# Kernel tuning notes

Hardware: AMD Instinct MI355X
Metric: run time of the kernel (lower is better)

## Reference

```python
import jax, jax.numpy as jnp
import numpy as np
import math

TABLE_SIZE = 524288      # 2**19 entries per level
NUM_LEVELS = 16
MIN_RES = 16
MAX_RES = 1024
FEATURE_DIM = 2
N_POINTS = 1 << 20
HASH_PRIME = np.uint32(2654435761)  # standard Instant-NGP spatial hash prime


def _hash(vertex, table_size, hash_offset):
    # vertex: (N, L, 2) int32 grid coords; returns (N, L) int32 table indices
    v = vertex.astype(jnp.uint32)
    h = v[..., 0] ^ (v[..., 1] * HASH_PRIME)          # uint32 wraparound mul
    return (h % jnp.uint32(table_size)).astype(jnp.int32) + hash_offset


def setup_inputs() -> dict:
    key = jax.random.key(0)
    kx, kt = jax.random.split(key)
    x = jax.random.uniform(kx, (N_POINTS, 2), dtype=jnp.float32)  # points in [0,1)^2
    # nn.initializers.uniform(scale=1e-4): U[0, 1e-4)
    hash_table = jax.random.uniform(
        kt, (TABLE_SIZE * NUM_LEVELS, FEATURE_DIM), dtype=jnp.float32) * 1e-4
    return {"x": x, "hash_table": hash_table}


def reference(x, hash_table):
    levels = jnp.arange(NUM_LEVELS)
    growth = math.exp((math.log(MAX_RES) - math.log(MIN_RES)) / (NUM_LEVELS - 1))
    scalings = jnp.floor(MIN_RES * (growth ** levels.astype(jnp.float32)))  # (L,)
    hash_offset = (levels * TABLE_SIZE).astype(jnp.int32)                   # (L,)

    scaled = x[:, None, :] * scalings[None, :, None]   # (N, L, 2)
    scaled_c = jnp.ceil(scaled).astype(jnp.int32)
    scaled_f = jnp.floor(scaled).astype(jnp.int32)
    off = scaled - scaled_f                            # (N, L, 2) bilinear weights

    v0 = scaled_c                                                          # (cx, cy)
    v1 = jnp.stack([scaled_c[..., 0], scaled_f[..., 1]], axis=-1)          # (cx, fy)
    v2 = jnp.stack([scaled_f[..., 0], scaled_c[..., 1]], axis=-1)          # (fx, cy)
    v3 = scaled_f                                                          # (fx, fy)

    f0 = hash_table[_hash(v0, TABLE_SIZE, hash_offset)]  # (N, L, F)
    f1 = hash_table[_hash(v1, TABLE_SIZE, hash_offset)]
    f2 = hash_table[_hash(v2, TABLE_SIZE, hash_offset)]
    f3 = hash_table[_hash(v3, TABLE_SIZE, hash_offset)]

    ox = off[..., 0:1]  # (N, L, 1)
    oy = off[..., 1:2]
    f03 = f0 * ox + f3 * (1.0 - ox)
    f12 = f1 * ox + f2 * (1.0 - ox)
    enc = f03 * oy + f12 * (1.0 - oy)                  # (N, L, F)
    # per-point layout matches ravel(transpose(F,L)->(L,F)): level-major
    return enc.reshape(x.shape[0], NUM_LEVELS * FEATURE_DIM)
```

## Files before the change

kernel.cpp:

```cpp
#include <hip/hip_runtime.h>

#define TS 524288u
#define PRIME 2654435761u
#define NPTS 1048576u
#define MASK (TS - 1u)
#define NBUK 4096u
#define CAP 320u
#define OVF_CAP 8192u

#define WS_CURSOR   0u
#define WS_OVFCNT   16384u
#define WS_OVF_XY   16640u
#define WS_OVF_IDX  82176u
#define WS_XYBUF    131072u
#define WS_IDXBUF   10616832u
#define WS_NEED     15859712u

typedef float vfloat4 __attribute__((ext_vector_type(4)));

__device__ __constant__ float c_scale[16] = {
    16.f, 21.f, 27.f, 36.f, 48.f, 64.f, 84.f, 111.f,
    147.f, 194.f, 256.f, 337.f, 445.f, 588.f, 776.f, 1024.f
};

#define W0 17
#define W1 22
#define W2 28
#define W3 37
#define B0 0
#define B1 (B0 + W0*W0)
#define B2 (B1 + W1*W1)
#define B3 (B2 + W2*W2)
#define NSTAGE (B3 + W3*W3)

__device__ __forceinline__ unsigned bucket_of(float2 xy) {
    unsigned bx = (unsigned)(xy.x * 64.0f); if (bx > 63u) bx = 63u;
    unsigned by = (unsigned)(xy.y * 64.0f); if (by > 63u) by = 63u;
    return by * 64u + bx;
}

__device__ __forceinline__ void enc_level(
    float2 xy, unsigned l, const float2* __restrict__ tab,
    float& ex, float& ey)
{
    float s = c_scale[l];
    float sx = xy.x * s, sy = xy.y * s;
    float fxf = floorf(sx), fyf = floorf(sy);
    float cxf = ceilf(sx),  cyf = ceilf(sy);
    float ox = sx - fxf, oy = sy - fyf;
    unsigned fx = (unsigned)(int)fxf, fy = (unsigned)(int)fyf;
    unsigned cx = (unsigned)(int)cxf, cy = (unsigned)(int)cyf;
    unsigned hcy = cy * PRIME, hfy = fy * PRIME;
    unsigned base = l << 19;
    float2 f0 = tab[((cx ^ hcy) & MASK) | base];
    float2 f1 = tab[((cx ^ hfy) & MASK) | base];
    float2 f2 = tab[((fx ^ hcy) & MASK) | base];
    float2 f3 = tab[((fx ^ hfy) & MASK) | base];
    float wox = 1.0f - ox, woy = 1.0f - oy;
    float f03x = f0.x * ox + f3.x * wox;
    float f03y = f0.y * ox + f3.y * wox;
    float f12x = f1.x * ox + f2.x * wox;
    float f12y = f1.y * ox + f2.y * wox;
    ex = f03x * oy + f12x * woy;
    ey = f03y * oy + f12y * woy;
}

__global__ __launch_bounds__(256) void init_kernel(
    unsigned* __restrict__ cursor, unsigned* __restrict__ ovf_cnt)
{
    unsigned t = blockIdx.x * 256u + threadIdx.x;
    if (t < NBUK) cursor[t] = t * CAP;
    if (t == 0u) *ovf_cnt = 0u;
}

__global__ __launch_bounds__(256) void sort_kernel(
    const float2* __restrict__ x,
    unsigned* __restrict__ cursor,
    unsigned* __restrict__ ovf_cnt,
    float2* __restrict__ ovf_xy,
    unsigned* __restrict__ ovf_idx,
    float2* __restrict__ xybuf,
    unsigned* __restrict__ idxbuf)
{
    __shared__ unsigned lhist[NBUK];
    __shared__ unsigned lbase_cap[NBUK];
    unsigned tid = threadIdx.x;
    unsigned cbase = blockIdx.x * 1024u;

    for (unsigned j = tid; j < NBUK; j += 256u) lhist[j] = 0u;
    __syncthreads();

    float2 pxy[4];
#pragma unroll
    for (int k = 0; k < 4; ++k) {
        float2 xy = x[cbase + tid + (unsigned)k * 256u];
        pxy[k] = xy;
        atomicAdd(&lhist[bucket_of(xy)], 1u);
    }
    __syncthreads();

    for (unsigned j = tid; j < NBUK; j += 256u) {
        unsigned c = lhist[j];
        unsigned base = 0u, take = 0u;
        if (c) {
            base = atomicAdd(&cursor[j], c);
            unsigned prior = base - j * CAP;
            unsigned avail = (prior >= CAP) ? 0u : (CAP - prior);
            take = (c < avail) ? c : avail;
        }
        lbase_cap[j] = (base << 9) | take;
        lhist[j] = 0u;
    }
    __syncthreads();

#pragma unroll
    for (int k = 0; k < 4; ++k) {
        float2 xy = pxy[k];
        unsigned b = bucket_of(xy);
        unsigned idx = cbase + tid + (unsigned)k * 256u;
        unsigned loff = atomicAdd(&lhist[b], 1u);
        unsigned bc = lbase_cap[b];
        unsigned take = bc & 511u;
        if (loff < take) {
            unsigned pos = (bc >> 9) + loff;
            xybuf[pos] = xy;
            idxbuf[pos] = idx;
        } else {
            unsigned o = atomicAdd(ovf_cnt, 1u);
            if (o < OVF_CAP) { ovf_xy[o] = xy; ovf_idx[o] = idx; }
        }
    }
}

__global__ __launch_bounds__(512) void encode_kernel(
    const float2* __restrict__ xybuf,
    const unsigned* __restrict__ idxbuf,
    const unsigned* __restrict__ cursor,
    const float2* __restrict__ tab,
    vfloat4* __restrict__ out)
{
    __shared__ float2 lds[NSTAGE];
    unsigned tid = threadIdx.x;

#define STAGE(L, W, B)                                                  \
    for (unsigned i = tid; i < (unsigned)((W)*(W)); i += 512u) {        \
        unsigned vy = i / (unsigned)(W), vx = i % (unsigned)(W);        \
        unsigned h = ((vx ^ (vy * PRIME)) & MASK) | ((unsigned)(L) << 19); \
        lds[(B) + i] = tab[h];                                          \
    }
    STAGE(0, W0, B0)
    STAGE(1, W1, B1)
    STAGE(2, W2, B2)
    STAGE(3, W3, B3)
#undef STAGE
    __syncthreads();

    unsigned wave = tid >> 6;
    unsigned lane = tid & 63u;
    unsigned lq   = lane & 3u;
    unsigned s0   = lane >> 2;
    unsigned b    = blockIdx.x * 8u + wave;
    unsigned total = cursor[b] - b * CAP;
    unsigned cnt  = (total < CAP) ? total : CAP;
    unsigned l0   = lq << 2;
    unsigned pbase = b * CAP;

    const unsigned Wk[4] = { W0, W1, W2, W3 };
    const unsigned Bk[4] = { B0, B1, B2, B3 };

    for (unsigned s = s0; s < cnt; s += 16u) {
        float2 xy   = xybuf[pbase + s];
        unsigned idx = idxbuf[pbase + s];
        vfloat4 r[2];

        if (lq == 0u) {
#pragma unroll
            for (int k = 0; k < 4; ++k) {
                float sc = c_scale[k];
                float sx = xy.x * sc, sy = xy.y * sc;
                float fxf = floorf(sx), fyf = floorf(sy);
                float cxf = ceilf(sx),  cyf = ceilf(sy);
                float ox = sx - fxf, oy = sy - fyf;
                unsigned fx = (unsigned)(int)fxf, fy = (unsigned)(int)fyf;
                unsigned cx = (unsigned)(int)cxf, cy = (unsigned)(int)cyf;
                unsigned w = Wk[k], bb = Bk[k];
                float2 f0 = lds[bb + cy * w + cx];
                float2 f1 = lds[bb + fy * w + cx];
                float2 f2 = lds[bb + cy * w + fx];
                float2 f3 = lds[bb + fy * w + fx];
                float wox = 1.0f - ox, woy = 1.0f - oy;
                float f03x = f0.x * ox + f3.x * wox;
                float f03y = f0.y * ox + f3.y * wox;
                float f12x = f1.x * ox + f2.x * wox;
                float f12y = f1.y * ox + f2.y * wox;
                float ex = f03x * oy + f12x * woy;
                float ey = f03y * oy + f12y * woy;
                if ((k & 1) == 0) { r[k >> 1].x = ex; r[k >> 1].y = ey; }
                else              { r[k >> 1].z = ex; r[k >> 1].w = ey; }
            }
        } else {
#pragma unroll
            for (int k = 0; k < 4; ++k) {
                float ex, ey;
                enc_level(xy, l0 + (unsigned)k, tab, ex, ey);
                if ((k & 1) == 0) { r[k >> 1].x = ex; r[k >> 1].y = ey; }
                else              { r[k >> 1].z = ex; r[k >> 1].w = ey; }
            }
        }

        unsigned o = idx * 8u + lq * 2u;
        __builtin_nontemporal_store(r[0], &out[o]);
        __builtin_nontemporal_store(r[1], &out[o + 1]);
    }
}

__global__ __launch_bounds__(256) void fixup_kernel(
    const unsigned* __restrict__ ovf_cnt,
    const float2* __restrict__ ovf_xy,
    const unsigned* __restrict__ ovf_idx,
    const float2* __restrict__ tab,
    vfloat4* __restrict__ out)
{
    unsigned n = *ovf_cnt; if (n > OVF_CAP) n = OVF_CAP;
    unsigned stride = gridDim.x * 256u;
    for (unsigned p = blockIdx.x * 256u + threadIdx.x; p < n; p += stride) {
        float2 xy = ovf_xy[p];
        unsigned idx = ovf_idx[p];
        vfloat4 acc[8];
#pragma unroll
        for (int l = 0; l < 16; ++l) {
            float ex, ey;
            enc_level(xy, (unsigned)l, tab, ex, ey);
            if ((l & 1) == 0) { acc[l >> 1].x = ex; acc[l >> 1].y = ey; }
            else              { acc[l >> 1].z = ex; acc[l >> 1].w = ey; }
        }
#pragma unroll
        for (int q = 0; q < 8; ++q) out[idx * 8u + (unsigned)q] = acc[q];
    }
}

__global__ __launch_bounds__(256) void hashenc_kernel(
    const float2* __restrict__ x,
    const float2* __restrict__ tab,
    vfloat4* __restrict__ out,
    unsigned pts_per_block)
{
    __shared__ float2 lds[NSTAGE];
    unsigned tid = threadIdx.x;

#define STAGE(L, W, B)                                                  \
    for (unsigned i = tid; i < (unsigned)((W)*(W)); i += 256u) {        \
        unsigned vy = i / (unsigned)(W), vx = i % (unsigned)(W);        \
        unsigned h = ((vx ^ (vy * PRIME)) & MASK) | ((unsigned)(L) << 19); \
        lds[(B) + i] = tab[h];                                          \
    }
    STAGE(0, W0, B0)
    STAGE(1, W1, B1)
    STAGE(2, W2, B2)
    STAGE(3, W3, B3)
#undef STAGE
    __syncthreads();

    const unsigned lq = tid & 3u;
    const unsigned lane_p = tid >> 2;
    const unsigned l0 = lq << 2;
    const unsigned bs = blockIdx.x * pts_per_block;
    unsigned be = bs + pts_per_block;
    if (be > NPTS) be = NPTS;

    const unsigned Wk[4] = { W0, W1, W2, W3 };
    const unsigned Bk[4] = { B0, B1, B2, B3 };

    for (unsigned p = bs + lane_p; p < be; p += 64u) {
        float2 xy = x[p];
        vfloat4 r[2];

        if (lq == 0u) {
#pragma unroll
            for (int k = 0; k < 4; ++k) {
                float s = c_scale[k];
                float sx = xy.x * s, sy = xy.y * s;
                float fxf = floorf(sx), fyf = floorf(sy);
                float cxf = ceilf(sx),  cyf = ceilf(sy);
                float ox = sx - fxf, oy = sy - fyf;
                unsigned fx = (unsigned)(int)fxf, fy = (unsigned)(int)fyf;
                unsigned cx = (unsigned)(int)cxf, cy = (unsigned)(int)cyf;
                unsigned w = Wk[k], b = Bk[k];
                float2 f0 = lds[b + cy * w + cx];
                float2 f1 = lds[b + fy * w + cx];
                float2 f2 = lds[b + cy * w + fx];
                float2 f3 = lds[b + fy * w + fx];
                float wox = 1.0f - ox, woy = 1.0f - oy;
                float f03x = f0.x * ox + f3.x * wox;
                float f03y = f0.y * ox + f3.y * wox;
                float f12x = f1.x * ox + f2.x * wox;
                float f12y = f1.y * ox + f2.y * wox;
                float ex = f03x * oy + f12x * woy;
                float ey = f03y * oy + f12y * woy;
                if ((k & 1) == 0) { r[k >> 1].x = ex; r[k >> 1].y = ey; }
                else              { r[k >> 1].z = ex; r[k >> 1].w = ey; }
            }
        } else {
#pragma unroll
            for (int k = 0; k < 4; ++k) {
                float ex, ey;
                enc_level(xy, l0 + (unsigned)k, tab, ex, ey);
                if ((k & 1) == 0) { r[k >> 1].x = ex; r[k >> 1].y = ey; }
                else              { r[k >> 1].z = ex; r[k >> 1].w = ey; }
            }
        }

        unsigned o = p * 8u + lq * 2u;
        __builtin_nontemporal_store(r[0], &out[o]);
        __builtin_nontemporal_store(r[1], &out[o + 1]);
    }
}

extern "C" void kernel_launch(void* const* d_in, const int* in_sizes, int n_in,
                              void* d_out, int out_size, void* d_ws, size_t ws_size,
                              hipStream_t stream)
{
    const float2* x   = (const float2*)d_in[0];
    const float2* tab = (const float2*)d_in[1];
    vfloat4* out = (vfloat4*)d_out;

    if (d_ws != nullptr && ws_size >= (size_t)WS_NEED) {
        char* ws = (char*)d_ws;
        unsigned* cursor  = (unsigned*)(ws + WS_CURSOR);
        unsigned* ovf_cnt = (unsigned*)(ws + WS_OVFCNT);
        float2*   ovf_xy  = (float2*)  (ws + WS_OVF_XY);
        unsigned* ovf_idx = (unsigned*)(ws + WS_OVF_IDX);
        float2*   xybuf   = (float2*)  (ws + WS_XYBUF);
        unsigned* idxbuf  = (unsigned*)(ws + WS_IDXBUF);

        init_kernel<<<16, 256, 0, stream>>>(cursor, ovf_cnt);
        sort_kernel<<<1024, 256, 0, stream>>>(x, cursor, ovf_cnt, ovf_xy,
                                              ovf_idx, xybuf, idxbuf);
        encode_kernel<<<NBUK / 8, 512, 0, stream>>>(xybuf, idxbuf, cursor, tab, out);
        fixup_kernel<<<8, 256, 0, stream>>>(ovf_cnt, ovf_xy, ovf_idx, tab, out);
    } else {
        const unsigned n_blocks = 1536u;
        const unsigned ppb = (NPTS + n_blocks - 1u) / n_blocks;
        hashenc_kernel<<<n_blocks, 256, 0, stream>>>(x, tab, out, ppb);
    }
}
```

Before: 314.1 us.

## Stage per-bucket hash tiles for all levels in LDS, enlarge sort blocks

Each wave in the encode kernel now gathers, for its own spatial bucket, the local window of hashed table entries for all 16 levels into LDS. All levels then interpolate from LDS instead of doing random global gathers, which previously happened for levels 4-15. The sort kernel also handles 4096 points per 512-thread block, cutting global cursor atomics. In exchange the staging gathers add upfront work per bucket and LDS use rises to about 65KB per block, which can lower occupancy.

```diff
diff --git a/kernel.cpp b/kernel.cpp
--- a/kernel.cpp
+++ b/kernel.cpp
@@ -22,6 +22,14 @@
     16.f, 21.f, 27.f, 36.f, 48.f, 64.f, 84.f, 111.f,
     147.f, 194.f, 256.f, 337.f, 445.f, 588.f, 776.f, 1024.f
 };
+
+__device__ __constant__ unsigned c_lvl[16] = {
+    (0u  <<5)|3u,  (9u  <<5)|3u,  (18u <<5)|3u,  (27u <<5)|3u,
+    (36u <<5)|3u,  (45u <<5)|3u,  (54u <<5)|4u,  (70u <<5)|4u,
+    (86u <<5)|5u,  (111u<<5)|6u,  (147u<<5)|6u,  (183u<<5)|8u,
+    (247u<<5)|9u,  (328u<<5)|12u, (472u<<5)|15u, (697u<<5)|18u
+};
+#define BUKSTRIDE 1021u
 
 #define W0 17
 #define W1 22
@@ -73,7 +81,7 @@
     if (t == 0u) *ovf_cnt = 0u;
 }
 
-__global__ __launch_bounds__(256) void sort_kernel(
+__global__ __launch_bounds__(512) void sort_kernel(
     const float2* __restrict__ x,
     unsigned* __restrict__ cursor,
     unsigned* __restrict__ ovf_cnt,
@@ -85,21 +93,21 @@
     __shared__ unsigned lhist[NBUK];
     __shared__ unsigned lbase_cap[NBUK];
     unsigned tid = threadIdx.x;
-    unsigned cbase = blockIdx.x * 1024u;
-
-    for (unsigned j = tid; j < NBUK; j += 256u) lhist[j] = 0u;
-    __syncthreads();
-
-    float2 pxy[4];
-#pragma unroll
-    for (int k = 0; k < 4; ++k) {
-        float2 xy = x[cbase + tid + (unsigned)k * 256u];
+    unsigned cbase = blockIdx.x * 4096u;
+
+    for (unsigned j = tid; j < NBUK; j += 512u) lhist[j] = 0u;
+    __syncthreads();
+
+    float2 pxy[8];
+#pragma unroll
+    for (int k = 0; k < 8; ++k) {
+        float2 xy = x[cbase + tid + (unsigned)k * 512u];
         pxy[k] = xy;
         atomicAdd(&lhist[bucket_of(xy)], 1u);
     }
     __syncthreads();
 
-    for (unsigned j = tid; j < NBUK; j += 256u) {
+    for (unsigned j = tid; j < NBUK; j += 512u) {
         unsigned c = lhist[j];
         unsigned base = 0u, take = 0u;
         if (c) {
@@ -114,10 +122,10 @@
     __syncthreads();
 
 #pragma unroll
-    for (int k = 0; k < 4; ++k) {
+    for (int k = 0; k < 8; ++k) {
         float2 xy = pxy[k];
         unsigned b = bucket_of(xy);
-        unsigned idx = cbase + tid + (unsigned)k * 256u;
+        unsigned idx = cbase + tid + (unsigned)k * 512u;
         unsigned loff = atomicAdd(&lhist[b], 1u);
         unsigned bc = lbase_cap[b];
         unsigned take = bc & 511u;
@@ -139,73 +147,75 @@
     const float2* __restrict__ tab,
     vfloat4* __restrict__ out)
 {
-    __shared__ float2 lds[NSTAGE];
-    unsigned tid = threadIdx.x;
-
-#define STAGE(L, W, B)                                                  \
-    for (unsigned i = tid; i < (unsigned)((W)*(W)); i += 512u) {        \
-        unsigned vy = i / (unsigned)(W), vx = i % (unsigned)(W);        \
-        unsigned h = ((vx ^ (vy * PRIME)) & MASK) | ((unsigned)(L) << 19); \
-        lds[(B) + i] = tab[h];                                          \
-    }
-    STAGE(0, W0, B0)
-    STAGE(1, W1, B1)
-    STAGE(2, W2, B2)
-    STAGE(3, W3, B3)
-#undef STAGE
-    __syncthreads();
-
+    __shared__ float2 lds[8u * BUKSTRIDE];
+    unsigned tid  = threadIdx.x;
     unsigned wave = tid >> 6;
     unsigned lane = tid & 63u;
-    unsigned lq   = lane & 3u;
-    unsigned s0   = lane >> 2;
     unsigned b    = blockIdx.x * 8u + wave;
+    unsigned bx   = b & 63u, by = b >> 6;
+    float bxf = (float)bx * 0.015625f;
+    float byf = (float)by * 0.015625f;
+    unsigned wbase = wave * BUKSTRIDE;
+
+    for (unsigned l = 0; l < 16u; ++l) {
+        float s = c_scale[l];
+        int x0 = (int)floorf(bxf * s);
+        int y0 = (int)floorf(byf * s);
+        unsigned u = c_lvl[l];
+        unsigned W = u & 31u;
+        unsigned base = wbase + (u >> 5);
+        unsigned n = W * W;
+        for (unsigned i = lane; i < n; i += 64u) {
+            unsigned vy = (unsigned)(y0 + (int)(i / W));
+            unsigned vx = (unsigned)(x0 + (int)(i % W));
+            unsigned h = ((vx ^ (vy * PRIME)) & MASK) | (l << 19);
+            lds[base + i] = tab[h];
+        }
+    }
+    __syncthreads();
+
+    unsigned lq = lane & 3u;
+    unsigned s0 = lane >> 2;
+    unsigned l0 = lq << 2;
     unsigned total = cursor[b] - b * CAP;
-    unsigned cnt  = (total < CAP) ? total : CAP;
-    unsigned l0   = lq << 2;
+    unsigned cnt = (total < CAP) ? total : CAP;
     unsigned pbase = b * CAP;
-
-    const unsigned Wk[4] = { W0, W1, W2, W3 };
-    const unsigned Bk[4] = { B0, B1, B2, B3 };
 
     for (unsigned s = s0; s < cnt; s += 16u) {
         float2 xy   = xybuf[pbase + s];
         unsigned idx = idxbuf[pbase + s];
         vfloat4 r[2];
 
-        if (lq == 0u) {
-#pragma unroll
-            for (int k = 0; k < 4; ++k) {
-                float sc = c_scale[k];
-                float sx = xy.x * sc, sy = xy.y * sc;
-                float fxf = floorf(sx), fyf = floorf(sy);
-                float cxf = ceilf(sx),  cyf = ceilf(sy);
-                float ox = sx - fxf, oy = sy - fyf;
-                unsigned fx = (unsigned)(int)fxf, fy = (unsigned)(int)fyf;
-                unsigned cx = (unsigned)(int)cxf, cy = (unsigned)(int)cyf;
-                unsigned w = Wk[k], bb = Bk[k];
-                float2 f0 = lds[bb + cy * w + cx];
-                float2 f1 = lds[bb + fy * w + cx];
-                float2 f2 = lds[bb + cy * w + fx];
-                float2 f3 = lds[bb + fy * w + fx];
-                float wox = 1.0f - ox, woy = 1.0f - oy;
-                float f03x = f0.x * ox + f3.x * wox;
-                float f03y = f0.y * ox + f3.y * wox;
-                float f12x = f1.x * ox + f2.x * wox;
-                float f12y = f1.y * ox + f2.y * wox;
-                float ex = f03x * oy + f12x * woy;
-                float ey = f03y * oy + f12y * woy;
-                if ((k & 1) == 0) { r[k >> 1].x = ex; r[k >> 1].y = ey; }
-                else              { r[k >> 1].z = ex; r[k >> 1].w = ey; }
-            }
-        } else {
-#pragma unroll
-            for (int k = 0; k < 4; ++k) {
-                float ex, ey;
-                enc_level(xy, l0 + (unsigned)k, tab, ex, ey);
-                if ((k & 1) == 0) { r[k >> 1].x = ex; r[k >> 1].y = ey; }
-                else              { r[k >> 1].z = ex; r[k >> 1].w = ey; }
-            }
+#pragma unroll
+        for (int k = 0; k < 4; ++k) {
+            unsigned l = l0 + (unsigned)k;
+            float sc = c_scale[l];
+            float sx = xy.x * sc, sy = xy.y * sc;
+            float fxf = floorf(sx), fyf = floorf(sy);
+            float cxf = ceilf(sx),  cyf = ceilf(sy);
+            float ox = sx - fxf, oy = sy - fyf;
+            int x0 = (int)floorf(bxf * sc);
+            int y0 = (int)floorf(byf * sc);
+            unsigned lxf = (unsigned)((int)fxf - x0);
+            unsigned lxc = (unsigned)((int)cxf - x0);
+            unsigned lyf = (unsigned)((int)fyf - y0);
+            unsigned lyc = (unsigned)((int)cyf - y0);
+            unsigned u = c_lvl[l];
+            unsigned W = u & 31u;
+            unsigned base = wbase + (u >> 5);
+            float2 f0 = lds[base + lyc * W + lxc];
+            float2 f1 = lds[base + lyf * W + lxc];
+            float2 f2 = lds[base + lyc * W + lxf];
+            float2 f3 = lds[base + lyf * W + lxf];
+            float wox = 1.0f - ox, woy = 1.0f - oy;
+            float f03x = f0.x * ox + f3.x * wox;
+            float f03y = f0.y * ox + f3.y * wox;
+            float f12x = f1.x * ox + f2.x * wox;
+            float f12y = f1.y * ox + f2.y * wox;
+            float ex = f03x * oy + f12x * woy;
+            float ey = f03y * oy + f12y * woy;
+            if ((k & 1) == 0) { r[k >> 1].x = ex; r[k >> 1].y = ey; }
+            else              { r[k >> 1].z = ex; r[k >> 1].w = ey; }
         }
 
         unsigned o = idx * 8u + lq * 2u;
@@ -334,8 +344,8 @@
         unsigned* idxbuf  = (unsigned*)(ws + WS_IDXBUF);
 
         init_kernel<<<16, 256, 0, stream>>>(cursor, ovf_cnt);
-        sort_kernel<<<1024, 256, 0, stream>>>(x, cursor, ovf_cnt, ovf_xy,
-                                              ovf_idx, xybuf, idxbuf);
+        sort_kernel<<<256, 512, 0, stream>>>(x, cursor, ovf_cnt, ovf_xy,
+                                             ovf_idx, xybuf, idxbuf);
         encode_kernel<<<NBUK / 8, 512, 0, stream>>>(xybuf, idxbuf, cursor, tab, out);
         fixup_kernel<<<8, 256, 0, stream>>>(ovf_cnt, ovf_xy, ovf_idx, tab, out);
     } else {
```

After: 254.7 us. 18.9% less time.
